# Kernel tuning notes

Measured on AMD Instinct MI355X. Metric: run time of the kernel, lower is better.

The kernel has to match this reference:

```python
import jax, jax.numpy as jnp
import numpy as np


def setup_inputs() -> dict:
    key = jax.random.key(0)
    ks = jax.random.split(key, 6)
    B, T, H = 32, 2048, 1024
    s_t = jax.random.normal(ks[0], (B, H), dtype=jnp.float32)
    prev_s = jax.random.normal(ks[1], (B, T, H), dtype=jnp.float32)
    scale = 1.0 / np.sqrt(H)
    W_prev = jax.random.normal(ks[2], (H, H), dtype=jnp.float32) * scale
    W_s = jax.random.normal(ks[3], (H, H), dtype=jnp.float32) * scale
    b_s = jax.random.normal(ks[4], (H,), dtype=jnp.float32) * scale
    v = jax.random.normal(ks[5], (H,), dtype=jnp.float32) * scale
    return {"s_t": s_t, "prev_s": prev_s, "W_prev": W_prev, "W_s": W_s, "b_s": b_s, "v": v}


def reference(s_t, prev_s, W_prev, W_s, b_s, v):
    # et = W_prev(prev_s) + (W_s(s_t) + b)[:, None, :]   -> [B, T, H]
    et = jnp.einsum('bth,dh->btd', prev_s, W_prev)
    dec_fea = jnp.einsum('bh,dh->bd', s_t, W_s) + b_s
    et = jnp.tanh(et + dec_fea[:, None, :])
    # scalar score per time step: v-projection -> [B, T]
    scores = jnp.einsum('bth,h->bt', et, v)
    at = jax.nn.softmax(scores, axis=1)
    # context: weighted sum over previous states -> [B, H]
    ct_d = jnp.einsum('bt,bth->bh', at, prev_s)
    prev_s_new = jnp.concatenate([prev_s, s_t[:, None, :]], axis=1)
    return ct_d, prev_s_new
```

## Files before the change

### kernel.cpp

```cpp
#include <hip/hip_runtime.h>
#include <hip/hip_bf16.h>
#include <stdint.h>

#define Bb 32
#define Tt 2048
#define Hh 1024

typedef __bf16 bf16;
typedef __bf16 bf16x8 __attribute__((ext_vector_type(8)));
typedef __bf16 bf16x4 __attribute__((ext_vector_type(4)));
typedef float  f32x4  __attribute__((ext_vector_type(4)));

__device__ __forceinline__ float tanh_fast(float x){
    float e = __expf(2.0f*x);
    return 1.0f - 2.0f/(e + 1.0f);
}

__device__ __forceinline__ void gl2lds16(const void* g, void* l){
    __builtin_amdgcn_global_load_lds(
        (const __attribute__((address_space(1))) uint32_t*)g,
        (__attribute__((address_space(3))) uint32_t*)l, 16, 0, 0);
}

__global__ __launch_bounds__(256) void k_copy_conv(
    const float* __restrict__ prev, float* __restrict__ outp, bf16* __restrict__ abf)
{
    long i = (long)blockIdx.x*256 + threadIdx.x;
    f32x4 v = __builtin_nontemporal_load(&((const f32x4*)prev)[i]);
    long b = i >> 19;
    __builtin_nontemporal_store(v, &((f32x4*)outp)[i + (b<<8)]);
    if (abf){
        bf16x4 h = { (bf16)v.x,(bf16)v.y,(bf16)v.z,(bf16)v.w };
        ((bf16x4*)abf)[i] = h;
    }
}

__global__ __launch_bounds__(256) void k_wconv(const float* __restrict__ w, bf16* __restrict__ wb)
{
    long i = (long)blockIdx.x*256 + threadIdx.x;
    f32x4 v = ((const f32x4*)w)[i];
    bf16x4 h = { (bf16)v.x,(bf16)v.y,(bf16)v.z,(bf16)v.w };
    ((bf16x4*)wb)[i] = h;
}

__global__ __launch_bounds__(256) void k_strow(const float* __restrict__ s_t, float* __restrict__ outp)
{
    int b = blockIdx.x;
    f32x4 v = ((const f32x4*)(s_t + (size_t)b*Hh))[threadIdx.x];
    ((f32x4*)(outp + (size_t)b*(Tt+1)*Hh + (size_t)Tt*Hh))[threadIdx.x] = v;
}

__global__ __launch_bounds__(256) void k_decfea(
    const float* __restrict__ s_t, const float* __restrict__ Ws,
    const float* __restrict__ bs, float* __restrict__ dec)
{
    int o = blockIdx.x*4 + (threadIdx.x>>6);
    int lane = threadIdx.x & 63;
    int b = o >> 10, d = o & 1023;
    const f32x4* sr = (const f32x4*)(s_t + (size_t)b*Hh);
    const f32x4* wr = (const f32x4*)(Ws  + (size_t)d*Hh);
    float sum = 0.f;
    #pragma unroll
    for (int it=0; it<4; ++it){
        f32x4 a = sr[it*64+lane], w = wr[it*64+lane];
        sum += a.x*w.x + a.y*w.y + a.z*w.z + a.w*w.w;
    }
    #pragma unroll
    for (int off=32; off>=1; off>>=1) sum += __shfl_xor(sum, off, 64);
    if (lane==0) dec[o] = sum + bs[d];
}

template<bool WS>
__global__ __launch_bounds__(256) void k_gemm_score(
    const bf16* __restrict__ Ab, const float* __restrict__ Af,
    const bf16* __restrict__ Wb, const float* __restrict__ Wf,
    const float* __restrict__ dec, const float* __restrict__ v,
    float* __restrict__ scores)
{
    __shared__ __align__(16) bf16 lA[2][128*64];
    __shared__ __align__(16) bf16 lB[2][128*64];
    __shared__ float rowsum[128];
    const int tid  = threadIdx.x;
    const int wave = tid>>6, lane = tid&63, quad = lane>>4, l15 = lane&15;
    const int wm = wave>>1, wn = wave&1;
    const int f = blockIdx.x;
    const int row0 = (((f>>6)<<3) + (f&7)) * 128;
    const int col0 = ((f>>3)&7) * 128;
    if (tid < 128) rowsum[tid] = 0.f;

    int Lm[4], Loct[4];
    #pragma unroll
    for (int it=0; it<4; ++it){ int L=it*256+tid; Lm[it]=L&127; Loct[it]=L>>7; }

    f32x4 acc[4][4] = {};

    auto stageW = [&](bf16* dA, bf16* dB, int kc){
        const int k0 = kc*64;
        #pragma unroll
        for (int it=0; it<4; ++it){
            int L = it*256+tid;
            gl2lds16(Ab + (size_t)(row0+Lm[it])*Hh + k0 + Loct[it]*8, dA + (size_t)L*8);
        }
        #pragma unroll
        for (int it=0; it<4; ++it){
            int L = it*256+tid;
            gl2lds16(Wb + (size_t)(col0+Lm[it])*Hh + k0 + Loct[it]*8, dB + (size_t)L*8);
        }
    };
    auto stageF = [&](bf16* dA, bf16* dB, int kc){
        const int k0 = kc*64;
        #pragma unroll
        for (int it=0; it<4; ++it){
            int L = it*256+tid;
            const f32x4* g = (const f32x4*)(Af + (size_t)(row0+Lm[it])*Hh + k0 + Loct[it]*8);
            f32x4 x0=g[0], x1=g[1];
            bf16x8 r = {(bf16)x0.x,(bf16)x0.y,(bf16)x0.z,(bf16)x0.w,
                        (bf16)x1.x,(bf16)x1.y,(bf16)x1.z,(bf16)x1.w};
            *(bf16x8*)(dA + (size_t)L*8) = r;
        }
        #pragma unroll
        for (int it=0; it<4; ++it){
            int L = it*256+tid;
            const f32x4* g = (const f32x4*)(Wf + (size_t)(col0+Lm[it])*Hh + k0 + Loct[it]*8);
            f32x4 x0=g[0], x1=g[1];
            bf16x8 r = {(bf16)x0.x,(bf16)x0.y,(bf16)x0.z,(bf16)x0.w,
                        (bf16)x1.x,(bf16)x1.y,(bf16)x1.z,(bf16)x1.w};
            *(bf16x8*)(dB + (size_t)L*8) = r;
        }
    };

    bf16 *cA = lA[0], *cB = lB[0], *nA = lA[1], *nB = lB[1];
    if (WS) stageW(cA, cB, 0); else stageF(cA, cB, 0);
    __syncthreads();

    for (int kc=0; kc<16; ++kc){
        if (kc < 15){ if (WS) stageW(nA, nB, kc+1); else stageF(nA, nB, kc+1); }
        #pragma unroll
        for (int ks=0; ks<2; ++ks){
            bf16x8 afr[4], bfr[4];
            const int ob = (ks*4+quad)*128;
            #pragma unroll
            for (int tr=0; tr<4; ++tr)
                afr[tr] = *(const bf16x8*)(cA + (size_t)(ob + wm*64 + tr*16 + l15)*8);
            #pragma unroll
            for (int tc=0; tc<4; ++tc)
                bfr[tc] = *(const bf16x8*)(cB + (size_t)(ob + wn*64 + tc*16 + l15)*8);
            #pragma unroll
            for (int tr=0; tr<4; ++tr)
                #pragma unroll
                for (int tc=0; tc<4; ++tc)
                    acc[tr][tc] = __builtin_amdgcn_mfma_f32_16x16x32_bf16(
                        afr[tr], bfr[tc], acc[tr][tc], 0, 0, 0);
        }
        __syncthreads();
        bf16* t;
        t = cA; cA = nA; nA = t;
        t = cB; cB = nB; nB = t;
    }

    const int b = row0 >> 11;
    float df[4], vv[4];
    #pragma unroll
    for (int tc=0; tc<4; ++tc){
        int d = col0 + wn*64 + tc*16 + l15;
        df[tc] = dec[b*Hh + d];
        vv[tc] = v[d];
    }
    #pragma unroll
    for (int tr=0; tr<4; ++tr){
        #pragma unroll
        for (int i=0; i<4; ++i){
            float p = 0.f;
            #pragma unroll
            for (int tc=0; tc<4; ++tc)
                p += vv[tc]*tanh_fast(acc[tr][tc][i] + df[tc]);
            p += __shfl_xor(p,1,64); p += __shfl_xor(p,2,64);
            p += __shfl_xor(p,4,64); p += __shfl_xor(p,8,64);
            if (l15==0) atomicAdd(&rowsum[wm*64 + tr*16 + quad*4 + i], p);
        }
    }
    __syncthreads();
    if (tid < 128)
        atomicAdd(&scores[(size_t)b*Tt + (row0 & (Tt-1)) + tid], rowsum[tid]);
}

__global__ __launch_bounds__(256) void k_softmax(const float* __restrict__ sc, float* __restrict__ at)
{
    __shared__ float red[4];
    const int b = blockIdx.x, tid = threadIdx.x;
    const int wave = tid>>6, lane = tid&63;
    float s[8]; float mx = -3.4e38f;
    #pragma unroll
    for (int i=0;i<8;++i){ s[i] = sc[(size_t)b*Tt + tid + i*256]; mx = fmaxf(mx, s[i]); }
    #pragma unroll
    for (int off=32; off>=1; off>>=1) mx = fmaxf(mx, __shfl_xor(mx, off, 64));
    if (lane==0) red[wave]=mx;
    __syncthreads();
    mx = fmaxf(fmaxf(red[0],red[1]), fmaxf(red[2],red[3]));
    float sum=0.f;
    #pragma unroll
    for (int i=0;i<8;++i){ s[i]=__expf(s[i]-mx); sum+=s[i]; }
    #pragma unroll
    for (int off=32; off>=1; off>>=1) sum += __shfl_xor(sum, off, 64);
    __syncthreads();
    if (lane==0) red[wave]=sum;
    __syncthreads();
    sum = red[0]+red[1]+red[2]+red[3];
    float inv = 1.0f/sum;
    #pragma unroll
    for (int i=0;i<8;++i) at[(size_t)b*Tt + tid + i*256] = s[i]*inv;
}

template<bool WS, bool PART>
__global__ __launch_bounds__(256) void k_ct(
    const bf16* __restrict__ Ab, const float* __restrict__ Af,
    const float* __restrict__ at, float* __restrict__ out)
{
    const int b = blockIdx.x, tcn = blockIdx.y, tid = threadIdx.x;
    float a0=0,a1=0,a2=0,a3=0;
    const int tBase = tcn*128;
    #pragma unroll 4
    for (int tt=0; tt<128; ++tt){
        int t = tBase+tt;
        float w = at[(size_t)b*Tt + t];
        if (WS){
            bf16x4 x = ((const bf16x4*)(Ab + ((size_t)b*Tt + t)*Hh))[tid];
            a0 += w*(float)x[0]; a1 += w*(float)x[1];
            a2 += w*(float)x[2]; a3 += w*(float)x[3];
        } else {
            f32x4 x = ((const f32x4*)(Af + ((size_t)b*Tt + t)*Hh))[tid];
            a0 += w*x.x; a1 += w*x.y; a2 += w*x.z; a3 += w*x.w;
        }
    }
    if (PART){
        f32x4 r = {a0,a1,a2,a3};
        ((f32x4*)(out + ((size_t)tcn*Bb + b)*Hh))[tid] = r;
    } else {
        float* o = out + (size_t)b*Hh + tid*4;
        atomicAdd(o+0,a0); atomicAdd(o+1,a1); atomicAdd(o+2,a2); atomicAdd(o+3,a3);
    }
}

__global__ __launch_bounds__(256) void k_ctred(const float* __restrict__ part, float* __restrict__ ct)
{
    const int b = blockIdx.x, tid = threadIdx.x;
    f32x4 s = {0.f,0.f,0.f,0.f};
    #pragma unroll
    for (int p=0;p<16;++p){
        f32x4 x = ((const f32x4*)(part + ((size_t)p*Bb + b)*Hh))[tid];
        s.x+=x.x; s.y+=x.y; s.z+=x.z; s.w+=x.w;
    }
    ((f32x4*)(ct + (size_t)b*Hh))[tid] = s;
}

extern "C" void kernel_launch(void* const* d_in, const int* in_sizes, int n_in,
                              void* d_out, int out_size, void* d_ws, size_t ws_size,
                              hipStream_t stream)
{
    const float* s_t  = (const float*)d_in[0];
    const float* prev = (const float*)d_in[1];
    const float* Wp   = (const float*)d_in[2];
    const float* Ws   = (const float*)d_in[3];
    const float* bs   = (const float*)d_in[4];
    const float* v    = (const float*)d_in[5];
    float* ct   = (float*)d_out;
    float* outp = ct + (size_t)Bb*Hh;

    char* ws = (char*)d_ws;
    const size_t ABF = (size_t)Bb*Tt*Hh*2;
    const size_t WBF = (size_t)Hh*Hh*2;
    const size_t SMALL = (size_t)(32768 + Bb*Tt + Bb*Tt)*4;
    const size_t CTP = (size_t)16*Bb*Hh*4;
    bool big   = ws_size >= ABF + WBF + SMALL;
    bool bigct = ws_size >= ABF + WBF + SMALL + CTP;

    bf16 *abf=nullptr, *wbf=nullptr;
    float *dec, *scores, *at, *ctp=nullptr;
    if (big){
        abf = (bf16*)ws; wbf = (bf16*)(ws + ABF);
        dec = (float*)(ws + ABF + WBF);
    } else {
        dec = (float*)ws;
    }
    scores = dec + 32768;
    at     = scores + (size_t)Bb*Tt;
    if (bigct) ctp = at + (size_t)Bb*Tt;

    hipMemsetAsync(d_out, 0, (size_t)Bb*Hh*4, stream);
    hipMemsetAsync((void*)scores, 0, (size_t)Bb*Tt*4, stream);

    k_copy_conv<<<65536,256,0,stream>>>(prev, outp, abf);
    if (big) k_wconv<<<1024,256,0,stream>>>(Wp, wbf);
    k_strow<<<Bb,256,0,stream>>>(s_t, outp);
    k_decfea<<<8192,256,0,stream>>>(s_t, Ws, bs, dec);
    if (big)
        k_gemm_score<true ><<<4096,256,0,stream>>>(abf, nullptr, wbf, nullptr, dec, v, scores);
    else
        k_gemm_score<false><<<4096,256,0,stream>>>(nullptr, prev, nullptr, Wp, dec, v, scores);
    k_softmax<<<Bb,256,0,stream>>>(scores, at);
    if (big){
        if (bigct){
            k_ct<true,true ><<<dim3(Bb,16),256,0,stream>>>(abf, nullptr, at, ctp);
            k_ctred<<<Bb,256,0,stream>>>(ctp, ct);
        } else {
            k_ct<true,false><<<dim3(Bb,16),256,0,stream>>>(abf, nullptr, at, ct);
        }
    } else {
        k_ct<false,false><<<dim3(Bb,16),256,0,stream>>>(nullptr, prev, at, ct);
    }
}
```

Baseline: 754.9 us.

## Swizzle GEMM LDS tiles row-major with XOR and replace score atomics with partials

```diff
diff --git a/kernel.cpp b/kernel.cpp
--- a/kernel.cpp
+++ b/kernel.cpp
@@ -75,7 +75,7 @@
     const bf16* __restrict__ Ab, const float* __restrict__ Af,
     const bf16* __restrict__ Wb, const float* __restrict__ Wf,
     const float* __restrict__ dec, const float* __restrict__ v,
-    float* __restrict__ scores)
+    float* __restrict__ scp)
 {
     __shared__ __align__(16) bf16 lA[2][128*64];
     __shared__ __align__(16) bf16 lB[2][128*64];
@@ -85,12 +85,9 @@
     const int wm = wave>>1, wn = wave&1;
     const int f = blockIdx.x;
     const int row0 = (((f>>6)<<3) + (f&7)) * 128;
-    const int col0 = ((f>>3)&7) * 128;
+    const int ct8 = (f>>3)&7;
+    const int col0 = ct8 * 128;
     if (tid < 128) rowsum[tid] = 0.f;
-
-    int Lm[4], Loct[4];
-    #pragma unroll
-    for (int it=0; it<4; ++it){ int L=it*256+tid; Lm[it]=L&127; Loct[it]=L>>7; }
 
     f32x4 acc[4][4] = {};
 
@@ -99,12 +96,16 @@
         #pragma unroll
         for (int it=0; it<4; ++it){
             int L = it*256+tid;
-            gl2lds16(Ab + (size_t)(row0+Lm[it])*Hh + k0 + Loct[it]*8, dA + (size_t)L*8);
+            int r = L>>3;
+            int oc = (L&7) ^ (r&7);
+            gl2lds16(Ab + (size_t)(row0+r)*Hh + k0 + oc*8, dA + (size_t)L*8);
         }
         #pragma unroll
         for (int it=0; it<4; ++it){
             int L = it*256+tid;
-            gl2lds16(Wb + (size_t)(col0+Lm[it])*Hh + k0 + Loct[it]*8, dB + (size_t)L*8);
+            int r = L>>3;
+            int oc = (L&7) ^ (r&7);
+            gl2lds16(Wb + (size_t)(col0+r)*Hh + k0 + oc*8, dB + (size_t)L*8);
         }
     };
     auto stageF = [&](bf16* dA, bf16* dB, int kc){
@@ -112,20 +113,22 @@
         #pragma unroll
         for (int it=0; it<4; ++it){
             int L = it*256+tid;
-            const f32x4* g = (const f32x4*)(Af + (size_t)(row0+Lm[it])*Hh + k0 + Loct[it]*8);
+            int r = L>>3, oc = L&7;
+            const f32x4* g = (const f32x4*)(Af + (size_t)(row0+r)*Hh + k0 + oc*8);
             f32x4 x0=g[0], x1=g[1];
-            bf16x8 r = {(bf16)x0.x,(bf16)x0.y,(bf16)x0.z,(bf16)x0.w,
-                        (bf16)x1.x,(bf16)x1.y,(bf16)x1.z,(bf16)x1.w};
-            *(bf16x8*)(dA + (size_t)L*8) = r;
+            bf16x8 rr = {(bf16)x0.x,(bf16)x0.y,(bf16)x0.z,(bf16)x0.w,
+                         (bf16)x1.x,(bf16)x1.y,(bf16)x1.z,(bf16)x1.w};
+            *(bf16x8*)(dA + ((size_t)r*8 + (oc ^ (r&7)))*8) = rr;
         }
         #pragma unroll
         for (int it=0; it<4; ++it){
             int L = it*256+tid;
-            const f32x4* g = (const f32x4*)(Wf + (size_t)(col0+Lm[it])*Hh + k0 + Loct[it]*8);
+            int r = L>>3, oc = L&7;
+            const f32x4* g = (const f32x4*)(Wf + (size_t)(col0+r)*Hh + k0 + oc*8);
             f32x4 x0=g[0], x1=g[1];
-            bf16x8 r = {(bf16)x0.x,(bf16)x0.y,(bf16)x0.z,(bf16)x0.w,
-                        (bf16)x1.x,(bf16)x1.y,(bf16)x1.z,(bf16)x1.w};
-            *(bf16x8*)(dB + (size_t)L*8) = r;
+            bf16x8 rr = {(bf16)x0.x,(bf16)x0.y,(bf16)x0.z,(bf16)x0.w,
+                         (bf16)x1.x,(bf16)x1.y,(bf16)x1.z,(bf16)x1.w};
+            *(bf16x8*)(dB + ((size_t)r*8 + (oc ^ (r&7)))*8) = rr;
         }
     };
 
@@ -138,13 +141,17 @@
         #pragma unroll
         for (int ks=0; ks<2; ++ks){
             bf16x8 afr[4], bfr[4];
-            const int ob = (ks*4+quad)*128;
+            const int ob = ks*4 + quad;
             #pragma unroll
-            for (int tr=0; tr<4; ++tr)
-                afr[tr] = *(const bf16x8*)(cA + (size_t)(ob + wm*64 + tr*16 + l15)*8);
+            for (int tr=0; tr<4; ++tr){
+                int r = wm*64 + tr*16 + l15;
+                afr[tr] = *(const bf16x8*)(cA + ((size_t)r*8 + (ob ^ (r&7)))*8);
+            }
             #pragma unroll
-            for (int tc=0; tc<4; ++tc)
-                bfr[tc] = *(const bf16x8*)(cB + (size_t)(ob + wn*64 + tc*16 + l15)*8);
+            for (int tc=0; tc<4; ++tc){
+                int r = wn*64 + tc*16 + l15;
+                bfr[tc] = *(const bf16x8*)(cB + ((size_t)r*8 + (ob ^ (r&7)))*8);
+            }
             #pragma unroll
             for (int tr=0; tr<4; ++tr)
                 #pragma unroll
@@ -181,17 +188,23 @@
     }
     __syncthreads();
     if (tid < 128)
-        atomicAdd(&scores[(size_t)b*Tt + (row0 & (Tt-1)) + tid], rowsum[tid]);
-}
-
-__global__ __launch_bounds__(256) void k_softmax(const float* __restrict__ sc, float* __restrict__ at)
+        scp[(size_t)ct8*Bb*Tt + (size_t)b*Tt + (row0 & (Tt-1)) + tid] = rowsum[tid];
+}
+
+__global__ __launch_bounds__(256) void k_softmax(const float* __restrict__ scp, float* __restrict__ at)
 {
     __shared__ float red[4];
     const int b = blockIdx.x, tid = threadIdx.x;
     const int wave = tid>>6, lane = tid&63;
     float s[8]; float mx = -3.4e38f;
     #pragma unroll
-    for (int i=0;i<8;++i){ s[i] = sc[(size_t)b*Tt + tid + i*256]; mx = fmaxf(mx, s[i]); }
+    for (int i=0;i<8;++i){
+        size_t idx = (size_t)b*Tt + tid + i*256;
+        float acc = 0.f;
+        #pragma unroll
+        for (int p=0;p<8;++p) acc += scp[(size_t)p*Bb*Tt + idx];
+        s[i] = acc; mx = fmaxf(mx, acc);
+    }
     #pragma unroll
     for (int off=32; off>=1; off>>=1) mx = fmaxf(mx, __shfl_xor(mx, off, 64));
     if (lane==0) red[wave]=mx;
@@ -269,35 +282,34 @@
     char* ws = (char*)d_ws;
     const size_t ABF = (size_t)Bb*Tt*Hh*2;
     const size_t WBF = (size_t)Hh*Hh*2;
-    const size_t SMALL = (size_t)(32768 + Bb*Tt + Bb*Tt)*4;
+    const size_t SMALL = (size_t)(32768 + 8*Bb*Tt + Bb*Tt)*4;
     const size_t CTP = (size_t)16*Bb*Hh*4;
     bool big   = ws_size >= ABF + WBF + SMALL;
     bool bigct = ws_size >= ABF + WBF + SMALL + CTP;
 
     bf16 *abf=nullptr, *wbf=nullptr;
-    float *dec, *scores, *at, *ctp=nullptr;
+    float *dec, *scp, *at, *ctp=nullptr;
     if (big){
         abf = (bf16*)ws; wbf = (bf16*)(ws + ABF);
         dec = (float*)(ws + ABF + WBF);
     } else {
         dec = (float*)ws;
     }
-    scores = dec + 32768;
-    at     = scores + (size_t)Bb*Tt;
+    scp = dec + 32768;
+    at  = scp + (size_t)8*Bb*Tt;
     if (bigct) ctp = at + (size_t)Bb*Tt;
 
     hipMemsetAsync(d_out, 0, (size_t)Bb*Hh*4, stream);
-    hipMemsetAsync((void*)scores, 0, (size_t)Bb*Tt*4, stream);
 
     k_copy_conv<<<65536,256,0,stream>>>(prev, outp, abf);
     if (big) k_wconv<<<1024,256,0,stream>>>(Wp, wbf);
     k_strow<<<Bb,256,0,stream>>>(s_t, outp);
     k_decfea<<<8192,256,0,stream>>>(s_t, Ws, bs, dec);
     if (big)
-        k_gemm_score<true ><<<4096,256,0,stream>>>(abf, nullptr, wbf, nullptr, dec, v, scores);
+        k_gemm_score<true ><<<4096,256,0,stream>>>(abf, nullptr, wbf, nullptr, dec, v, scp);
     else
-        k_gemm_score<false><<<4096,256,0,stream>>>(nullptr, prev, nullptr, Wp, dec, v, scores);
-    k_softmax<<<Bb,256,0,stream>>>(scores, at);
+        k_gemm_score<false><<<4096,256,0,stream>>>(nullptr, prev, nullptr, Wp, dec, v, scp);
+    k_softmax<<<Bb,256,0,stream>>>(scp, at);
     if (big){
         if (bigct){
             k_ct<true,true ><<<dim3(Bb,16),256,0,stream>>>(abf, nullptr, at, ctp);
```

Result: faster. 653.3 us (-13.5%).
